# Optimization experiments

Measured on AMD Instinct MI355X. Metric: run time of the kernel, lower is better.

Reference implementation:

```python
import jax, jax.numpy as jnp
import numpy as np

BATCH, T, IN, HID = 64, 2048, 128, 256

def setup_inputs() -> dict:
    key = jax.random.key(0)
    ks = jax.random.split(key, 6)
    s = 0.05
    return {
        "x": jax.random.normal(ks[0], (BATCH, T, IN), dtype=jnp.float32),
        "w_ih0": jax.random.normal(ks[1], (IN, 4 * HID), dtype=jnp.float32) * s,
        "w_hh0": jax.random.normal(ks[2], (HID, 4 * HID), dtype=jnp.float32) * s,
        "b0": jnp.zeros((4 * HID,), dtype=jnp.float32),
        "w_ih1": jax.random.normal(ks[3], (HID, 4 * HID), dtype=jnp.float32) * s,
        "w_hh1": jax.random.normal(ks[4], (HID, 4 * HID), dtype=jnp.float32) * s,
        "b1": jnp.zeros((4 * HID,), dtype=jnp.float32),
    }

def _run_layer(xs, h0, c0, w_ih, w_hh, b):
    # xs: [T, B, D]. Original code iterates input_[T-1-t], i.e. reversed time.
    def step(carry, xt):
        h, c = carry
        gates = xt @ w_ih + h @ w_hh + b            # [B, 4H]
        f, i, o, g = jnp.split(gates, 4, axis=1)     # split order f,i,o,g as in source
        c1 = jax.nn.sigmoid(f) * c + jax.nn.sigmoid(i) * jnp.tanh(g)
        h1 = jax.nn.sigmoid(o) * jnp.tanh(c1)
        return (h1, c1), h1
    (hT, cT), ys = jax.lax.scan(step, (h0, c0), xs[::-1])
    return ys, hT, cT

def reference(x, w_ih0, w_hh0, b0, w_ih1, w_hh1, b1):
    xs = jnp.transpose(x, (1, 0, 2))                 # batch_first -> [T, B, IN]
    B = xs.shape[1]
    H = w_hh0.shape[0]
    h0 = jnp.zeros((B, H), dtype=xs.dtype)
    # Both layers start from the SAME zero hx (faithful to source).
    y0, hn0, cn0 = _run_layer(xs, h0, h0, w_ih0, w_hh0, b0)
    y1, hn1, cn1 = _run_layer(y0, h0, h0, w_ih1, w_hh1, b1)
    # Source never transposes output back: output is [T, B, H]
    return y1, (jnp.stack([hn0, hn1], 0), jnp.stack([cn0, cn1], 0))
```

## Files before the change

kernel.cpp:

```cpp
#include <hip/hip_runtime.h>
#include <cstdint>
#include <cstddef>

#define T_STEPS 2048
#define NBATCH  64
#define HID     256
#define NGATE   1024

#define REC_LDS_BYTES (128*1024 + 8192 + 1024)

typedef _Float16 f16x8 __attribute__((ext_vector_type(8)));
typedef _Float16 h2f   __attribute__((ext_vector_type(2)));
typedef float    f32x4 __attribute__((ext_vector_type(4)));
typedef unsigned short u16x4 __attribute__((ext_vector_type(4)));

__device__ __forceinline__ unsigned short f2h_bits(float f) {
    _Float16 h = (_Float16)f;
    return __builtin_bit_cast(unsigned short, h);
}
__device__ __forceinline__ float h2f_scalar(unsigned short u) {
    return (float)__builtin_bit_cast(_Float16, u);
}

__device__ __forceinline__ float fdot2u(unsigned int hh, unsigned int ww, float acc) {
#if __has_builtin(__builtin_amdgcn_fdot2)
    return __builtin_amdgcn_fdot2(__builtin_bit_cast(h2f, hh),
                                  __builtin_bit_cast(h2f, ww), acc, false);
#else
    h2f a = __builtin_bit_cast(h2f, hh), b = __builtin_bit_cast(h2f, ww);
    return acc + (float)a.x * (float)b.x + (float)a.y * (float)b.y;
#endif
}

#define OFF_G    ((size_t)0)
#define OFF_Y0   ((size_t)268435456)
#define OFF_RW0  ((size_t)335544320)
#define OFF_RW1  ((size_t)335937536)
#define OFF_LF0  ((size_t)336330752)
#define OFF_LF1  ((size_t)336461824)
#define OFF_BS0  ((size_t)336592896)
#define OFF_BS1  ((size_t)336855040)
#define WS_NEED  ((size_t)337379328)

__global__ void convert_weights(const float* __restrict__ w_ih0, const float* __restrict__ w_hh0,
                                const float* __restrict__ w_ih1, const float* __restrict__ w_hh1,
                                unsigned short* __restrict__ RW0, unsigned short* __restrict__ RW1,
                                unsigned short* __restrict__ LF0, unsigned short* __restrict__ LF1,
                                unsigned short* __restrict__ BS0, unsigned short* __restrict__ BS1)
{
    int gid = blockIdx.x * blockDim.x + threadIdx.x;
    int gsz = gridDim.x * blockDim.x;
    for (int s = gid; s < 196608; s += gsz) {
        int i = s & 7;
        int t = s >> 3;
        int slot = t & 511;
        int q = t >> 9;
        int g = q / 12, c = q % 12;
        int l = slot & 63, wv = slot >> 6;
        int kh = wv & 1, ug = wv >> 1;
        int jp = c * 4 + (i >> 1);
        int k = kh * 128 + jp * 2 + (i & 1);
        int col = g * 256 + ug * 64 + l;
        RW0[s] = f2h_bits(w_hh0[k * 1024 + col]);
        RW1[s] = f2h_bits(w_hh1[k * 1024 + col]);
    }
    for (int s = gid; s < 65536; s += gsz) {
        int i = s & 7;
        int t = s >> 3;
        int slot = t & 511;
        int r = t >> 9;
        int g = r >> 2, cc = r & 3;
        int l = slot & 63, wv = slot >> 6;
        int kh = wv & 1, ug = wv >> 1;
        int jp = 48 + cc * 4 + (i >> 1);
        int k = kh * 128 + jp * 2 + (i & 1);
        int col = g * 256 + ug * 64 + l;
        LF0[s] = f2h_bits(w_hh0[k * 1024 + col]);
        LF1[s] = f2h_bits(w_hh1[k * 1024 + col]);
    }
    for (int s = gid; s < 131072; s += gsz) {
        int i = s & 7, lane = (s >> 3) & 63, kb = (s >> 9) & 3, n16 = s >> 11;
        int k = kb * 32 + (lane >> 4) * 8 + i;
        int n = n16 * 16 + (lane & 15);
        BS0[s] = f2h_bits(w_ih0[k * 1024 + n]);
    }
    for (int s = gid; s < 262144; s += gsz) {
        int i = s & 7, lane = (s >> 3) & 63, kb = (s >> 9) & 7, n16 = s >> 12;
        int k = kb * 32 + (lane >> 4) * 8 + i;
        int n = n16 * 16 + (lane & 15);
        BS1[s] = f2h_bits(w_ih1[k * 1024 + n]);
    }
}

template <int KB, int LAYER>
__global__ __launch_bounds__(256) void gemm_in(const float* __restrict__ A32,
                                               const unsigned short* __restrict__ A16,
                                               const unsigned short* __restrict__ Bsw,
                                               const float* __restrict__ bias,
                                               unsigned short* __restrict__ Gout)
{
    const int lane = threadIdx.x & 63;
    const int wave = threadIdx.x >> 6;
    const int nblk = blockIdx.x & 15;
    const int rblk = blockIdx.x >> 4;
    const int r0 = rblk * 128 + wave * 32;
    const int quad = lane >> 4, ln = lane & 15;

    f32x4 acc[2][4];
#pragma unroll
    for (int q = 0; q < 4; q++) {
        float bv = bias[(nblk * 4 + q) * 16 + ln];
#pragma unroll
        for (int mt = 0; mt < 2; mt++) {
            acc[mt][q][0] = bv; acc[mt][q][1] = bv; acc[mt][q][2] = bv; acc[mt][q][3] = bv;
        }
    }
    const int ar0 = r0 + ln, ar1 = r0 + 16 + ln;
    size_t aoff0, aoff1;
    if (LAYER == 0) {
        aoff0 = ((size_t)(ar0 & 63) * 2048 + (size_t)(2047 - (ar0 >> 6))) * 128;
        aoff1 = ((size_t)(ar1 & 63) * 2048 + (size_t)(2047 - (ar1 >> 6))) * 128;
    } else {
        aoff0 = ((size_t)(2047 - (ar0 >> 6)) * 64 + (size_t)(ar0 & 63)) * 256;
        aoff1 = ((size_t)(2047 - (ar1 >> 6)) * 64 + (size_t)(ar1 & 63)) * 256;
    }
#pragma unroll
    for (int kb = 0; kb < KB; kb++) {
        const int k0 = kb * 32 + quad * 8;
        f16x8 a0, a1;
        if (LAYER == 0) {
            const float* p0 = A32 + aoff0 + k0;
            const float* p1 = A32 + aoff1 + k0;
            float4 fa = *(const float4*)(p0);
            float4 fb = *(const float4*)(p0 + 4);
            float4 fc = *(const float4*)(p1);
            float4 fd = *(const float4*)(p1 + 4);
            a0[0] = (_Float16)fa.x; a0[1] = (_Float16)fa.y; a0[2] = (_Float16)fa.z; a0[3] = (_Float16)fa.w;
            a0[4] = (_Float16)fb.x; a0[5] = (_Float16)fb.y; a0[6] = (_Float16)fb.z; a0[7] = (_Float16)fb.w;
            a1[0] = (_Float16)fc.x; a1[1] = (_Float16)fc.y; a1[2] = (_Float16)fc.z; a1[3] = (_Float16)fc.w;
            a1[4] = (_Float16)fd.x; a1[5] = (_Float16)fd.y; a1[6] = (_Float16)fd.z; a1[7] = (_Float16)fd.w;
        } else {
            a0 = *(const f16x8*)(A16 + aoff0 + k0);
            a1 = *(const f16x8*)(A16 + aoff1 + k0);
        }
#pragma unroll
        for (int q = 0; q < 4; q++) {
            f16x8 bq = *(const f16x8*)(Bsw + (((size_t)(nblk * 4 + q) * KB + kb) * 64 + lane) * 8);
            acc[0][q] = __builtin_amdgcn_mfma_f32_16x16x32_f16(a0, bq, acc[0][q], 0, 0, 0);
            acc[1][q] = __builtin_amdgcn_mfma_f32_16x16x32_f16(a1, bq, acc[1][q], 0, 0, 0);
        }
    }
#pragma unroll
    for (int mt = 0; mt < 2; mt++)
#pragma unroll
        for (int q = 0; q < 4; q++)
#pragma unroll
            for (int rg = 0; rg < 4; rg++) {
                int row = r0 + mt * 16 + quad * 4 + rg;
                int col = (nblk * 4 + q) * 16 + ln;
                int swz = ((col & 255) << 2) | (col >> 8);
                Gout[(size_t)row * 1024 + swz] = f2h_bits(acc[mt][q][rg]);
            }
}

template <int LAYER>
__global__ __launch_bounds__(512, 2) void lstm_rec(const unsigned short* __restrict__ G,
                                                   const unsigned short* __restrict__ RW,
                                                   const unsigned short* __restrict__ LF,
                                                   unsigned short* __restrict__ Y0,
                                                   float* __restrict__ Out)
{
    extern __shared__ char smem[];
    uint4*  lds_w  = (uint4*)smem;
    float4* pb     = (float4*)(smem + 131072);
    unsigned short* lds_h0 = (unsigned short*)(smem + 131072 + 8192);
    unsigned short* lds_h1 = lds_h0 + 256;

    const int b = blockIdx.x;
    const int tid = threadIdx.x;
    const int wv = tid >> 6, l = tid & 63;
    const int kh = wv & 1;
    const int ug = wv >> 1;
    const int m = ug * 64 + l;

    uint4 rw[4][12];
#pragma unroll
    for (int g = 0; g < 4; ++g)
#pragma unroll
        for (int c = 0; c < 12; ++c)
            rw[g][c] = *(const uint4*)(RW + ((size_t)((g * 12 + c) * 512) + tid) * 8);

    {
        const uint4* src = (const uint4*)LF;
        for (int i = tid; i < 8192; i += 512) lds_w[i] = src[i];
    }
    if (tid < 256) lds_h0[tid] = 0;
    float c_state = 0.f, hprev = 0.f;
    __syncthreads();

    const u16x4* Gp = (const u16x4*)G;
    const size_t gbase = (size_t)b * 256 + m;
    u16x4 gp = Gp[gbase];

    for (int t = 0; t < T_STEPS; ++t) {
        const uint4* hv4 = (const uint4*)((t & 1) ? lds_h1 : lds_h0);
        uint4 hq = hv4[kh * 16 + (l & 15)];

        const int tn = (t + 1 < T_STEPS) ? t + 1 : t;
        u16x4 gpn = Gp[(size_t)tn * 16384 + gbase];

        if (t && kh == 0) {
            if (LAYER == 0) Y0[((size_t)(t - 1) * 64 + b) * 256 + m] = f2h_bits(hprev);
            else            Out[((size_t)(t - 1) * 64 + b) * 256 + m] = hprev;
        }

        unsigned hx = hq.x, hy = hq.y, hz = hq.z, hw = hq.w;
        unsigned sh[64];
#pragma unroll
        for (int q = 0; q < 16; ++q) {
            sh[q * 4 + 0] = __builtin_amdgcn_readlane(hx, q);
            sh[q * 4 + 1] = __builtin_amdgcn_readlane(hy, q);
            sh[q * 4 + 2] = __builtin_amdgcn_readlane(hz, q);
            sh[q * 4 + 3] = __builtin_amdgcn_readlane(hw, q);
        }

        float acc[4] = {0.f, 0.f, 0.f, 0.f};
#pragma unroll
        for (int c = 0; c < 12; ++c) {
#pragma unroll
            for (int g = 0; g < 4; ++g) {
                uint4 w = rw[g][c];
                acc[g] = fdot2u(sh[c * 4 + 0], w.x, acc[g]);
                acc[g] = fdot2u(sh[c * 4 + 1], w.y, acc[g]);
                acc[g] = fdot2u(sh[c * 4 + 2], w.z, acc[g]);
                acc[g] = fdot2u(sh[c * 4 + 3], w.w, acc[g]);
            }
        }
#pragma unroll
        for (int cc = 0; cc < 4; ++cc) {
#pragma unroll
            for (int g = 0; g < 4; ++g) {
                uint4 w = lds_w[(g * 4 + cc) * 512 + tid];
                acc[g] = fdot2u(sh[48 + cc * 4 + 0], w.x, acc[g]);
                acc[g] = fdot2u(sh[48 + cc * 4 + 1], w.y, acc[g]);
                acc[g] = fdot2u(sh[48 + cc * 4 + 2], w.z, acc[g]);
                acc[g] = fdot2u(sh[48 + cc * 4 + 3], w.w, acc[g]);
            }
        }

        float4 pv; pv.x = acc[0]; pv.y = acc[1]; pv.z = acc[2]; pv.w = acc[3];
        pb[tid] = pv;
        __syncthreads();
        float4 pp = pb[tid ^ 64];

        float fg = h2f_scalar(gp[0]) + (acc[0] + pp.x);
        float ig = h2f_scalar(gp[1]) + (acc[1] + pp.y);
        float og = h2f_scalar(gp[2]) + (acc[2] + pp.z);
        float gg = h2f_scalar(gp[3]) + (acc[3] + pp.w);

        float sf = 1.f / (1.f + __expf(-fg));
        float si = 1.f / (1.f + __expf(-ig));
        float so = 1.f / (1.f + __expf(-og));
        float tg = 1.f - 2.f / (1.f + __expf(2.f * gg));
        c_state = sf * c_state + si * tg;
        float tc = 1.f - 2.f / (1.f + __expf(2.f * c_state));
        float h = so * tc;
        hprev = h;

        unsigned short* hn = (t & 1) ? lds_h0 : lds_h1;
        if (kh == 0) hn[m] = f2h_bits(h);
        gp = gpn;
        __syncthreads();
    }
    if (kh == 0) {
        if (LAYER == 0) Y0[((size_t)(T_STEPS - 1) * 64 + b) * 256 + m] = f2h_bits(hprev);
        else            Out[((size_t)(T_STEPS - 1) * 64 + b) * 256 + m] = hprev;
        Out[(size_t)33554432 + (size_t)LAYER * 16384 + (size_t)b * 256 + m] = hprev;
        Out[(size_t)33554432 + 32768 + (size_t)LAYER * 16384 + (size_t)b * 256 + m] = c_state;
    }
}

extern "C" void kernel_launch(void* const* d_in, const int* in_sizes, int n_in,
                              void* d_out, int out_size, void* d_ws, size_t ws_size,
                              hipStream_t stream)
{
    const float* x     = (const float*)d_in[0];
    const float* w_ih0 = (const float*)d_in[1];
    const float* w_hh0 = (const float*)d_in[2];
    const float* b0    = (const float*)d_in[3];
    const float* w_ih1 = (const float*)d_in[4];
    const float* w_hh1 = (const float*)d_in[5];
    const float* b1    = (const float*)d_in[6];
    float* out = (float*)d_out;

    if (ws_size < WS_NEED) return;

    char* ws = (char*)d_ws;
    unsigned short* G   = (unsigned short*)(ws + OFF_G);
    unsigned short* Y0  = (unsigned short*)(ws + OFF_Y0);
    unsigned short* RW0 = (unsigned short*)(ws + OFF_RW0);
    unsigned short* RW1 = (unsigned short*)(ws + OFF_RW1);
    unsigned short* LF0 = (unsigned short*)(ws + OFF_LF0);
    unsigned short* LF1 = (unsigned short*)(ws + OFF_LF1);
    unsigned short* BS0 = (unsigned short*)(ws + OFF_BS0);
    unsigned short* BS1 = (unsigned short*)(ws + OFF_BS1);

    (void)hipFuncSetAttribute(reinterpret_cast<const void*>(&lstm_rec<0>),
                              hipFuncAttributeMaxDynamicSharedMemorySize, REC_LDS_BYTES);
    (void)hipFuncSetAttribute(reinterpret_cast<const void*>(&lstm_rec<1>),
                              hipFuncAttributeMaxDynamicSharedMemorySize, REC_LDS_BYTES);

    convert_weights<<<1024, 256, 0, stream>>>(w_ih0, w_hh0, w_ih1, w_hh1,
                                              RW0, RW1, LF0, LF1, BS0, BS1);
    gemm_in<4, 0><<<16384, 256, 0, stream>>>(x, nullptr, BS0, b0, G);
    lstm_rec<0><<<64, 512, REC_LDS_BYTES, stream>>>(G, RW0, LF0, Y0, out);
    gemm_in<8, 1><<<16384, 256, 0, stream>>>(nullptr, Y0, BS1, b1, G);
    lstm_rec<1><<<64, 512, REC_LDS_BYTES, stream>>>(G, RW1, LF1, Y0, out);
}
```

Measured before the change: 7.957 ms.

## Stream recurrent weight tail from global/L2 instead of LDS and remap gate columns

Reorganizes the recurrent weight layout so each lane covers two hidden units with paired gates, with the two halves of the gate set exchanged by a cross-lane shuffle. The weight tail that did not fit in registers moves out of LDS. It is now reloaded from global memory (L2-resident) every step in a double-buffered prefetch, which removes the 128KB LDS footprint. The hidden vector is read directly from LDS as uint4 instead of broadcast via readlane into scalar registers. The aim is to cut LDS usage and the readlane SALU overhead. The cost is per-step global loads on the serial critical path and extra shuffles.

```diff
diff --git a/kernel.cpp b/kernel.cpp
--- a/kernel.cpp
+++ b/kernel.cpp
@@ -7,12 +7,11 @@
 #define HID     256
 #define NGATE   1024
 
-#define REC_LDS_BYTES (128*1024 + 8192 + 1024)
+#define REC_LDS_BYTES (8192 + 1024)
 
 typedef _Float16 f16x8 __attribute__((ext_vector_type(8)));
 typedef _Float16 h2f   __attribute__((ext_vector_type(2)));
 typedef float    f32x4 __attribute__((ext_vector_type(4)));
-typedef unsigned short u16x4 __attribute__((ext_vector_type(4)));
 
 __device__ __forceinline__ unsigned short f2h_bits(float f) {
     _Float16 h = (_Float16)f;
@@ -34,49 +33,52 @@
 
 #define OFF_G    ((size_t)0)
 #define OFF_Y0   ((size_t)268435456)
-#define OFF_RW0  ((size_t)335544320)
-#define OFF_RW1  ((size_t)335937536)
-#define OFF_LF0  ((size_t)336330752)
-#define OFF_LF1  ((size_t)336461824)
+#define OFF_WR0  ((size_t)335544320)
+#define OFF_WR1  ((size_t)335872000)
+#define OFF_WG0  ((size_t)336199680)
+#define OFF_WG1  ((size_t)336396288)
 #define OFF_BS0  ((size_t)336592896)
 #define OFF_BS1  ((size_t)336855040)
 #define WS_NEED  ((size_t)337379328)
 
 __global__ void convert_weights(const float* __restrict__ w_ih0, const float* __restrict__ w_hh0,
                                 const float* __restrict__ w_ih1, const float* __restrict__ w_hh1,
-                                unsigned short* __restrict__ RW0, unsigned short* __restrict__ RW1,
-                                unsigned short* __restrict__ LF0, unsigned short* __restrict__ LF1,
+                                unsigned short* __restrict__ WR0, unsigned short* __restrict__ WR1,
+                                unsigned short* __restrict__ WG0, unsigned short* __restrict__ WG1,
                                 unsigned short* __restrict__ BS0, unsigned short* __restrict__ BS1)
 {
     int gid = blockIdx.x * blockDim.x + threadIdx.x;
     int gsz = gridDim.x * blockDim.x;
-    for (int s = gid; s < 196608; s += gsz) {
+    for (int s = gid; s < 163840; s += gsz) {
         int i = s & 7;
         int t = s >> 3;
         int slot = t & 511;
-        int q = t >> 9;
-        int g = q / 12, c = q % 12;
+        int ci = t >> 9;
+        int cx = ci / 10, c = ci % 10;
         int l = slot & 63, wv = slot >> 6;
-        int kh = wv & 1, ug = wv >> 1;
-        int jp = c * 4 + (i >> 1);
-        int k = kh * 128 + jp * 2 + (i & 1);
-        int col = g * 256 + ug * 64 + l;
-        RW0[s] = f2h_bits(w_hh0[k * 1024 + col]);
-        RW1[s] = f2h_bits(w_hh1[k * 1024 + col]);
-    }
-    for (int s = gid; s < 65536; s += gsz) {
+        int kh = wv & 1, lw = wv >> 1;
+        int upper = l >> 5, lu = l & 31;
+        int unit = lw * 64 + lu + ((cx >= 2) ? 32 : 0);
+        int j = unit + upper * 512 + (cx & 1) * 256;
+        int k = kh * 128 + (c * 4 + (i >> 1)) * 2 + (i & 1);
+        WR0[s] = f2h_bits(w_hh0[k * 1024 + j]);
+        WR1[s] = f2h_bits(w_hh1[k * 1024 + j]);
+    }
+    for (int s = gid; s < 98304; s += gsz) {
         int i = s & 7;
         int t = s >> 3;
         int slot = t & 511;
-        int r = t >> 9;
-        int g = r >> 2, cc = r & 3;
+        int ti = t >> 9;
+        int cx = ti / 6, cc = ti % 6;
+        int c = 10 + cc;
         int l = slot & 63, wv = slot >> 6;
-        int kh = wv & 1, ug = wv >> 1;
-        int jp = 48 + cc * 4 + (i >> 1);
-        int k = kh * 128 + jp * 2 + (i & 1);
-        int col = g * 256 + ug * 64 + l;
-        LF0[s] = f2h_bits(w_hh0[k * 1024 + col]);
-        LF1[s] = f2h_bits(w_hh1[k * 1024 + col]);
+        int kh = wv & 1, lw = wv >> 1;
+        int upper = l >> 5, lu = l & 31;
+        int unit = lw * 64 + lu + ((cx >= 2) ? 32 : 0);
+        int j = unit + upper * 512 + (cx & 1) * 256;
+        int k = kh * 128 + (c * 4 + (i >> 1)) * 2 + (i & 1);
+        WG0[s] = f2h_bits(w_hh0[k * 1024 + j]);
+        WG1[s] = f2h_bits(w_hh1[k * 1024 + j]);
     }
     for (int s = gid; s < 131072; s += gsz) {
         int i = s & 7, lane = (s >> 3) & 63, kb = (s >> 9) & 3, n16 = s >> 11;
@@ -165,118 +167,192 @@
 
 template <int LAYER>
 __global__ __launch_bounds__(512, 2) void lstm_rec(const unsigned short* __restrict__ G,
-                                                   const unsigned short* __restrict__ RW,
-                                                   const unsigned short* __restrict__ LF,
+                                                   const unsigned short* __restrict__ WR,
+                                                   const unsigned short* __restrict__ WG,
                                                    unsigned short* __restrict__ Y0,
                                                    float* __restrict__ Out)
 {
     extern __shared__ char smem[];
-    uint4*  lds_w  = (uint4*)smem;
-    float4* pb     = (float4*)(smem + 131072);
-    unsigned short* lds_h0 = (unsigned short*)(smem + 131072 + 8192);
+    float4* pb = (float4*)smem;
+    unsigned short* lds_h0 = (unsigned short*)(smem + 8192);
     unsigned short* lds_h1 = lds_h0 + 256;
 
     const int b = blockIdx.x;
     const int tid = threadIdx.x;
     const int wv = tid >> 6, l = tid & 63;
     const int kh = wv & 1;
-    const int ug = wv >> 1;
-    const int m = ug * 64 + l;
-
-    uint4 rw[4][12];
-#pragma unroll
-    for (int g = 0; g < 4; ++g)
-#pragma unroll
-        for (int c = 0; c < 12; ++c)
-            rw[g][c] = *(const uint4*)(RW + ((size_t)((g * 12 + c) * 512) + tid) * 8);
-
-    {
-        const uint4* src = (const uint4*)LF;
-        for (int i = tid; i < 8192; i += 512) lds_w[i] = src[i];
-    }
+    const int lw = wv >> 1;
+    const int upper = l >> 5, lu = l & 31;
+    const int u0 = lw * 64 + lu;
+    const int u1 = u0 + 32;
+
+    uint4 wr[4][10];
+#pragma unroll
+    for (int cx = 0; cx < 4; ++cx)
+#pragma unroll
+        for (int c = 0; c < 10; ++c)
+            wr[cx][c] = *(const uint4*)(WR + ((size_t)((cx * 10 + c) * 512) + tid) * 8);
+
+    const uint4* WGp = (const uint4*)WG;
+
     if (tid < 256) lds_h0[tid] = 0;
-    float c_state = 0.f, hprev = 0.f;
+    float c0s = 0.f, c1s = 0.f, hp0 = 0.f, hp1 = 0.f;
     __syncthreads();
 
-    const u16x4* Gp = (const u16x4*)G;
-    const size_t gbase = (size_t)b * 256 + m;
-    u16x4 gp = Gp[gbase];
+    const unsigned int* Gb = (const unsigned int*)G + (size_t)b * 512;
+    const int gi0 = u0 * 2 + upper, gi1 = u1 * 2 + upper;
+    unsigned int gp0 = Gb[gi0];
+    unsigned int gp1 = Gb[gi1];
 
     for (int t = 0; t < T_STEPS; ++t) {
+        const int tn = (t + 1 < T_STEPS) ? t + 1 : t;
+        unsigned int gp0n = Gb[(size_t)tn * 32768 + gi0];
+        unsigned int gp1n = Gb[(size_t)tn * 32768 + gi1];
+
+        uint4 tg0[4], tg1[4];
+#pragma unroll
+        for (int cx = 0; cx < 4; ++cx) tg0[cx] = WGp[(cx * 6 + 0) * 512 + tid];
+#pragma unroll
+        for (int cx = 0; cx < 4; ++cx) tg1[cx] = WGp[(cx * 6 + 1) * 512 + tid];
+
+        if (t && kh == 0 && upper == 0) {
+            if (LAYER == 0) {
+                Y0[((size_t)(t - 1) * 64 + b) * 256 + u0] = f2h_bits(hp0);
+                Y0[((size_t)(t - 1) * 64 + b) * 256 + u1] = f2h_bits(hp1);
+            } else {
+                Out[((size_t)(t - 1) * 64 + b) * 256 + u0] = hp0;
+                Out[((size_t)(t - 1) * 64 + b) * 256 + u1] = hp1;
+            }
+        }
+
         const uint4* hv4 = (const uint4*)((t & 1) ? lds_h1 : lds_h0);
-        uint4 hq = hv4[kh * 16 + (l & 15)];
-
-        const int tn = (t + 1 < T_STEPS) ? t + 1 : t;
-        u16x4 gpn = Gp[(size_t)tn * 16384 + gbase];
-
-        if (t && kh == 0) {
-            if (LAYER == 0) Y0[((size_t)(t - 1) * 64 + b) * 256 + m] = f2h_bits(hprev);
-            else            Out[((size_t)(t - 1) * 64 + b) * 256 + m] = hprev;
-        }
-
-        unsigned hx = hq.x, hy = hq.y, hz = hq.z, hw = hq.w;
-        unsigned sh[64];
-#pragma unroll
-        for (int q = 0; q < 16; ++q) {
-            sh[q * 4 + 0] = __builtin_amdgcn_readlane(hx, q);
-            sh[q * 4 + 1] = __builtin_amdgcn_readlane(hy, q);
-            sh[q * 4 + 2] = __builtin_amdgcn_readlane(hz, q);
-            sh[q * 4 + 3] = __builtin_amdgcn_readlane(hw, q);
-        }
-
-        float acc[4] = {0.f, 0.f, 0.f, 0.f};
-#pragma unroll
-        for (int c = 0; c < 12; ++c) {
-#pragma unroll
-            for (int g = 0; g < 4; ++g) {
-                uint4 w = rw[g][c];
-                acc[g] = fdot2u(sh[c * 4 + 0], w.x, acc[g]);
-                acc[g] = fdot2u(sh[c * 4 + 1], w.y, acc[g]);
-                acc[g] = fdot2u(sh[c * 4 + 2], w.z, acc[g]);
-                acc[g] = fdot2u(sh[c * 4 + 3], w.w, acc[g]);
+        float a0 = 0.f, a1 = 0.f, a2 = 0.f, a3 = 0.f;
+
+#pragma unroll
+        for (int c = 0; c < 10; ++c) {
+            uint4 h4 = hv4[kh * 16 + c];
+            uint4 w;
+            w = wr[0][c];
+            a0 = fdot2u(h4.x, w.x, a0); a0 = fdot2u(h4.y, w.y, a0);
+            a0 = fdot2u(h4.z, w.z, a0); a0 = fdot2u(h4.w, w.w, a0);
+            w = wr[1][c];
+            a1 = fdot2u(h4.x, w.x, a1); a1 = fdot2u(h4.y, w.y, a1);
+            a1 = fdot2u(h4.z, w.z, a1); a1 = fdot2u(h4.w, w.w, a1);
+            w = wr[2][c];
+            a2 = fdot2u(h4.x, w.x, a2); a2 = fdot2u(h4.y, w.y, a2);
+            a2 = fdot2u(h4.z, w.z, a2); a2 = fdot2u(h4.w, w.w, a2);
+            w = wr[3][c];
+            a3 = fdot2u(h4.x, w.x, a3); a3 = fdot2u(h4.y, w.y, a3);
+            a3 = fdot2u(h4.z, w.z, a3); a3 = fdot2u(h4.w, w.w, a3);
+        }
+#pragma unroll
+        for (int cc = 0; cc < 6; ++cc) {
+            const int c = 10 + cc;
+            uint4 h4 = hv4[kh * 16 + c];
+            if ((cc & 1) == 0) {
+                uint4 w;
+                w = tg0[0];
+                a0 = fdot2u(h4.x, w.x, a0); a0 = fdot2u(h4.y, w.y, a0);
+                a0 = fdot2u(h4.z, w.z, a0); a0 = fdot2u(h4.w, w.w, a0);
+                w = tg0[1];
+                a1 = fdot2u(h4.x, w.x, a1); a1 = fdot2u(h4.y, w.y, a1);
+                a1 = fdot2u(h4.z, w.z, a1); a1 = fdot2u(h4.w, w.w, a1);
+                w = tg0[2];
+                a2 = fdot2u(h4.x, w.x, a2); a2 = fdot2u(h4.y, w.y, a2);
+                a2 = fdot2u(h4.z, w.z, a2); a2 = fdot2u(h4.w, w.w, a2);
+                w = tg0[3];
+                a3 = fdot2u(h4.x, w.x, a3); a3 = fdot2u(h4.y, w.y, a3);
+                a3 = fdot2u(h4.z, w.z, a3); a3 = fdot2u(h4.w, w.w, a3);
+                if (cc + 2 < 6) {
+#pragma unroll
+                    for (int cx = 0; cx < 4; ++cx)
+                        tg0[cx] = WGp[(cx * 6 + cc + 2) * 512 + tid];
+                }
+            } else {
+                uint4 w;
+                w = tg1[0];
+                a0 = fdot2u(h4.x, w.x, a0); a0 = fdot2u(h4.y, w.y, a0);
+                a0 = fdot2u(h4.z, w.z, a0); a0 = fdot2u(h4.w, w.w, a0);
+                w = tg1[1];
+                a1 = fdot2u(h4.x, w.x, a1); a1 = fdot2u(h4.y, w.y, a1);
+                a1 = fdot2u(h4.z, w.z, a1); a1 = fdot2u(h4.w, w.w, a1);
+                w = tg1[2];
+                a2 = fdot2u(h4.x, w.x, a2); a2 = fdot2u(h4.y, w.y, a2);
+                a2 = fdot2u(h4.z, w.z, a2); a2 = fdot2u(h4.w, w.w, a2);
+                w = tg1[3];
+                a3 = fdot2u(h4.x, w.x, a3); a3 = fdot2u(h4.y, w.y, a3);
+                a3 = fdot2u(h4.z, w.z, a3); a3 = fdot2u(h4.w, w.w, a3);
+                if (cc + 2 < 6) {
+#pragma unroll
+                    for (int cx = 0; cx < 4; ++cx)
+                        tg1[cx] = WGp[(cx * 6 + cc + 2) * 512 + tid];
+                }
             }
         }
-#pragma unroll
-        for (int cc = 0; cc < 4; ++cc) {
-#pragma unroll
-            for (int g = 0; g < 4; ++g) {
-                uint4 w = lds_w[(g * 4 + cc) * 512 + tid];
-                acc[g] = fdot2u(sh[48 + cc * 4 + 0], w.x, acc[g]);
-                acc[g] = fdot2u(sh[48 + cc * 4 + 1], w.y, acc[g]);
-                acc[g] = fdot2u(sh[48 + cc * 4 + 2], w.z, acc[g]);
-                acc[g] = fdot2u(sh[48 + cc * 4 + 3], w.w, acc[g]);
-            }
-        }
-
-        float4 pv; pv.x = acc[0]; pv.y = acc[1]; pv.z = acc[2]; pv.w = acc[3];
+
+        float4 pv; pv.x = a0; pv.y = a1; pv.z = a2; pv.w = a3;
         pb[tid] = pv;
         __syncthreads();
         float4 pp = pb[tid ^ 64];
 
-        float fg = h2f_scalar(gp[0]) + (acc[0] + pp.x);
-        float ig = h2f_scalar(gp[1]) + (acc[1] + pp.y);
-        float og = h2f_scalar(gp[2]) + (acc[2] + pp.z);
-        float gg = h2f_scalar(gp[3]) + (acc[3] + pp.w);
-
-        float sf = 1.f / (1.f + __expf(-fg));
-        float si = 1.f / (1.f + __expf(-ig));
-        float so = 1.f / (1.f + __expf(-og));
-        float tg = 1.f - 2.f / (1.f + __expf(2.f * gg));
-        c_state = sf * c_state + si * tg;
-        float tc = 1.f - 2.f / (1.f + __expf(2.f * c_state));
-        float h = so * tc;
-        hprev = h;
+        float s0 = a0 + pp.x, s1 = a1 + pp.y;
+        float s2 = a2 + pp.z, s3 = a3 + pp.w;
+
+        {
+            float v0 = h2f_scalar((unsigned short)(gp0 & 0xffff)) + s0;
+            float v1 = h2f_scalar((unsigned short)(gp0 >> 16)) + s1;
+            float q0 = __shfl_xor(v0, 32, 64);
+            float q1 = __shfl_xor(v1, 32, 64);
+            float fg = upper ? q0 : v0;
+            float ig = upper ? q1 : v1;
+            float og = upper ? v0 : q0;
+            float gg = upper ? v1 : q1;
+            float sf = 1.f / (1.f + __expf(-fg));
+            float si = 1.f / (1.f + __expf(-ig));
+            float so = 1.f / (1.f + __expf(-og));
+            float tg = 1.f - 2.f / (1.f + __expf(2.f * gg));
+            c0s = sf * c0s + si * tg;
+            float tc = 1.f - 2.f / (1.f + __expf(2.f * c0s));
+            hp0 = so * tc;
+        }
+        {
+            float v0 = h2f_scalar((unsigned short)(gp1 & 0xffff)) + s2;
+            float v1 = h2f_scalar((unsigned short)(gp1 >> 16)) + s3;
+            float q0 = __shfl_xor(v0, 32, 64);
+            float q1 = __shfl_xor(v1, 32, 64);
+            float fg = upper ? q0 : v0;
+            float ig = upper ? q1 : v1;
+            float og = upper ? v0 : q0;
+            float gg = upper ? v1 : q1;
+            float sf = 1.f / (1.f + __expf(-fg));
+            float si = 1.f / (1.f + __expf(-ig));
+            float so = 1.f / (1.f + __expf(-og));
+            float tg = 1.f - 2.f / (1.f + __expf(2.f * gg));
+            c1s = sf * c1s + si * tg;
+            float tc = 1.f - 2.f / (1.f + __expf(2.f * c1s));
+            hp1 = so * tc;
+        }
 
         unsigned short* hn = (t & 1) ? lds_h0 : lds_h1;
-        if (kh == 0) hn[m] = f2h_bits(h);
-        gp = gpn;
+        if (kh == 0 && upper == 0) {
+            hn[u0] = f2h_bits(hp0);
+            hn[u1] = f2h_bits(hp1);
+        }
+        gp0 = gp0n; gp1 = gp1n;
         __syncthreads();
     }
-    if (kh == 0) {
-        if (LAYER == 0) Y0[((size_t)(T_STEPS - 1) * 64 + b) * 256 + m] = f2h_bits(hprev);
-        else            Out[((size_t)(T_STEPS - 1) * 64 + b) * 256 + m] = hprev;
-        Out[(size_t)33554432 + (size_t)LAYER * 16384 + (size_t)b * 256 + m] = hprev;
-        Out[(size_t)33554432 + 32768 + (size_t)LAYER * 16384 + (size_t)b * 256 + m] = c_state;
+    if (kh == 0 && upper == 0) {
+        if (LAYER == 0) {
+            Y0[((size_t)(T_STEPS - 1) * 64 + b) * 256 + u0] = f2h_bits(hp0);
+            Y0[((size_t)(T_STEPS - 1) * 64 + b) * 256 + u1] = f2h_bits(hp1);
+        } else {
+            Out[((size_t)(T_STEPS - 1) * 64 + b) * 256 + u0] = hp0;
+            Out[((size_t)(T_STEPS - 1) * 64 + b) * 256 + u1] = hp1;
+        }
+        Out[(size_t)33554432 + (size_t)LAYER * 16384 + (size_t)b * 256 + u0] = hp0;
+        Out[(size_t)33554432 + (size_t)LAYER * 16384 + (size_t)b * 256 + u1] = hp1;
+        Out[(size_t)33554432 + 32768 + (size_t)LAYER * 16384 + (size_t)b * 256 + u0] = c0s;
+        Out[(size_t)33554432 + 32768 + (size_t)LAYER * 16384 + (size_t)b * 256 + u1] = c1s;
     }
 }
 
@@ -298,10 +374,10 @@
     char* ws = (char*)d_ws;
     unsigned short* G   = (unsigned short*)(ws + OFF_G);
     unsigned short* Y0  = (unsigned short*)(ws + OFF_Y0);
-    unsigned short* RW0 = (unsigned short*)(ws + OFF_RW0);
-    unsigned short* RW1 = (unsigned short*)(ws + OFF_RW1);
-    unsigned short* LF0 = (unsigned short*)(ws + OFF_LF0);
-    unsigned short* LF1 = (unsigned short*)(ws + OFF_LF1);
+    unsigned short* WR0 = (unsigned short*)(ws + OFF_WR0);
+    unsigned short* WR1 = (unsigned short*)(ws + OFF_WR1);
+    unsigned short* WG0 = (unsigned short*)(ws + OFF_WG0);
+    unsigned short* WG1 = (unsigned short*)(ws + OFF_WG1);
     unsigned short* BS0 = (unsigned short*)(ws + OFF_BS0);
     unsigned short* BS1 = (unsigned short*)(ws + OFF_BS1);
 
@@ -311,9 +387,9 @@
                               hipFuncAttributeMaxDynamicSharedMemorySize, REC_LDS_BYTES);
 
     convert_weights<<<1024, 256, 0, stream>>>(w_ih0, w_hh0, w_ih1, w_hh1,
-                                              RW0, RW1, LF0, LF1, BS0, BS1);
+                                              WR0, WR1, WG0, WG1, BS0, BS1);
     gemm_in<4, 0><<<16384, 256, 0, stream>>>(x, nullptr, BS0, b0, G);
-    lstm_rec<0><<<64, 512, REC_LDS_BYTES, stream>>>(G, RW0, LF0, Y0, out);
+    lstm_rec<0><<<64, 512, REC_LDS_BYTES, stream>>>(G, WR0, WG0, Y0, out);
     gemm_in<8, 1><<<16384, 256, 0, stream>>>(nullptr, Y0, BS1, b1, G);
-    lstm_rec<1><<<64, 512, REC_LDS_BYTES, stream>>>(G, RW1, LF1, Y0, out);
-}
+    lstm_rec<1><<<64, 512, REC_LDS_BYTES, stream>>>(G, WR1, WG1, Y0, out);
+}
```

Result: slower. 17.38 ms (+118.4%).

## Halve recurrent block to 256 threads with 8 gate columns per thread

Applied to the files above, without the earlier changes.

Restructures the recurrent LSTM kernel from 512 to 256 threads per block. Each thread now computes partial dot products for two hidden units (8 gate columns) over half of K. It holds twice as many weights in registers (8x12 uint4) and reads h directly from LDS as uint4 instead of broadcasting via readlane. The partial sums are exchanged through two LDS buffers and every thread finishes one unit. This aims to cut per-step readlane overhead and give every thread output work, at the cost of much higher register pressure with one wave per SIMD, and twice the LDS weight reads per thread.

```diff
diff --git a/kernel.cpp b/kernel.cpp
--- a/kernel.cpp
+++ b/kernel.cpp
@@ -7,6 +7,7 @@
 #define HID     256
 #define NGATE   1024
 
+#define RC 12
 #define REC_LDS_BYTES (128*1024 + 8192 + 1024)
 
 typedef _Float16 f16x8 __attribute__((ext_vector_type(8)));
@@ -34,8 +35,8 @@
 
 #define OFF_G    ((size_t)0)
 #define OFF_Y0   ((size_t)268435456)
-#define OFF_RW0  ((size_t)335544320)
-#define OFF_RW1  ((size_t)335937536)
+#define OFF_WR0  ((size_t)335544320)
+#define OFF_WR1  ((size_t)335937536)
 #define OFF_LF0  ((size_t)336330752)
 #define OFF_LF1  ((size_t)336461824)
 #define OFF_BS0  ((size_t)336592896)
@@ -44,7 +45,7 @@
 
 __global__ void convert_weights(const float* __restrict__ w_ih0, const float* __restrict__ w_hh0,
                                 const float* __restrict__ w_ih1, const float* __restrict__ w_hh1,
-                                unsigned short* __restrict__ RW0, unsigned short* __restrict__ RW1,
+                                unsigned short* __restrict__ WR0, unsigned short* __restrict__ WR1,
                                 unsigned short* __restrict__ LF0, unsigned short* __restrict__ LF1,
                                 unsigned short* __restrict__ BS0, unsigned short* __restrict__ BS1)
 {
@@ -53,30 +54,32 @@
     for (int s = gid; s < 196608; s += gsz) {
         int i = s & 7;
         int t = s >> 3;
-        int slot = t & 511;
-        int q = t >> 9;
-        int g = q / 12, c = q % 12;
-        int l = slot & 63, wv = slot >> 6;
-        int kh = wv & 1, ug = wv >> 1;
-        int jp = c * 4 + (i >> 1);
-        int k = kh * 128 + jp * 2 + (i & 1);
-        int col = g * 256 + ug * 64 + l;
-        RW0[s] = f2h_bits(w_hh0[k * 1024 + col]);
-        RW1[s] = f2h_bits(w_hh1[k * 1024 + col]);
+        int tid = t & 255;
+        int ci = t >> 8;
+        int c = ci % 12, cx = ci / 12;
+        int gate = cx & 3, us = cx >> 2;
+        int wv = tid >> 6, l = tid & 63;
+        int kh = wv >> 1, ug = wv & 1;
+        int unit = ug * 128 + us * 64 + l;
+        int j = gate * 256 + unit;
+        int k = kh * 128 + (c * 4 + (i >> 1)) * 2 + (i & 1);
+        WR0[s] = f2h_bits(w_hh0[k * 1024 + j]);
+        WR1[s] = f2h_bits(w_hh1[k * 1024 + j]);
     }
     for (int s = gid; s < 65536; s += gsz) {
         int i = s & 7;
         int t = s >> 3;
-        int slot = t & 511;
-        int r = t >> 9;
-        int g = r >> 2, cc = r & 3;
-        int l = slot & 63, wv = slot >> 6;
-        int kh = wv & 1, ug = wv >> 1;
-        int jp = 48 + cc * 4 + (i >> 1);
-        int k = kh * 128 + jp * 2 + (i & 1);
-        int col = g * 256 + ug * 64 + l;
-        LF0[s] = f2h_bits(w_hh0[k * 1024 + col]);
-        LF1[s] = f2h_bits(w_hh1[k * 1024 + col]);
+        int tid = t & 255;
+        int idx = t >> 8;
+        int cc = idx & 3, cx = idx >> 2;
+        int gate = cx & 3, us = cx >> 2;
+        int wv = tid >> 6, l = tid & 63;
+        int kh = wv >> 1, ug = wv & 1;
+        int unit = ug * 128 + us * 64 + l;
+        int j = gate * 256 + unit;
+        int k = kh * 128 + ((12 + cc) * 4 + (i >> 1)) * 2 + (i & 1);
+        LF0[s] = f2h_bits(w_hh0[k * 1024 + j]);
+        LF1[s] = f2h_bits(w_hh1[k * 1024 + j]);
     }
     for (int s = gid; s < 131072; s += gsz) {
         int i = s & 7, lane = (s >> 3) & 63, kb = (s >> 9) & 3, n16 = s >> 11;
@@ -164,120 +167,151 @@
 }
 
 template <int LAYER>
-__global__ __launch_bounds__(512, 2) void lstm_rec(const unsigned short* __restrict__ G,
-                                                   const unsigned short* __restrict__ RW,
+__global__ __launch_bounds__(256, 1) void lstm_rec(const unsigned short* __restrict__ G,
+                                                   const unsigned short* __restrict__ WR,
                                                    const unsigned short* __restrict__ LF,
                                                    unsigned short* __restrict__ Y0,
                                                    float* __restrict__ Out)
 {
     extern __shared__ char smem[];
-    uint4*  lds_w  = (uint4*)smem;
-    float4* pb     = (float4*)(smem + 131072);
+    uint4*  lds_w = (uint4*)smem;
+    float4* pb_a  = (float4*)(smem + 131072);
+    float4* pb_b  = (float4*)(smem + 131072 + 4096);
     unsigned short* lds_h0 = (unsigned short*)(smem + 131072 + 8192);
     unsigned short* lds_h1 = lds_h0 + 256;
 
     const int b = blockIdx.x;
     const int tid = threadIdx.x;
     const int wv = tid >> 6, l = tid & 63;
-    const int kh = wv & 1;
-    const int ug = wv >> 1;
-    const int m = ug * 64 + l;
-
-    uint4 rw[4][12];
-#pragma unroll
-    for (int g = 0; g < 4; ++g)
-#pragma unroll
-        for (int c = 0; c < 12; ++c)
-            rw[g][c] = *(const uint4*)(RW + ((size_t)((g * 12 + c) * 512) + tid) * 8);
+    const int kh = wv >> 1;
+    const int ug = wv & 1;
+    const int mu = ug * 128 + kh * 64 + l;
+
+    uint4 wr[8][RC];
+#pragma unroll
+    for (int cx = 0; cx < 8; ++cx)
+#pragma unroll
+        for (int c = 0; c < RC; ++c)
+            wr[cx][c] = *(const uint4*)(WR + ((size_t)(cx * RC + c) * 256 + tid) * 8);
 
     {
         const uint4* src = (const uint4*)LF;
-        for (int i = tid; i < 8192; i += 512) lds_w[i] = src[i];
-    }
-    if (tid < 256) lds_h0[tid] = 0;
-    float c_state = 0.f, hprev = 0.f;
+        for (int i = tid; i < 8192; i += 256) lds_w[i] = src[i];
+    }
+    lds_h0[tid] = 0;
+    float c_state = 0.f, hlast = 0.f;
     __syncthreads();
 
     const u16x4* Gp = (const u16x4*)G;
-    const size_t gbase = (size_t)b * 256 + m;
+    const size_t gbase = (size_t)b * 256 + mu;
     u16x4 gp = Gp[gbase];
 
     for (int t = 0; t < T_STEPS; ++t) {
-        const uint4* hv4 = (const uint4*)((t & 1) ? lds_h1 : lds_h0);
-        uint4 hq = hv4[kh * 16 + (l & 15)];
-
         const int tn = (t + 1 < T_STEPS) ? t + 1 : t;
-        u16x4 gpn = Gp[(size_t)tn * 16384 + gbase];
-
-        if (t && kh == 0) {
-            if (LAYER == 0) Y0[((size_t)(t - 1) * 64 + b) * 256 + m] = f2h_bits(hprev);
-            else            Out[((size_t)(t - 1) * 64 + b) * 256 + m] = hprev;
-        }
-
-        unsigned hx = hq.x, hy = hq.y, hz = hq.z, hw = hq.w;
-        unsigned sh[64];
-#pragma unroll
-        for (int q = 0; q < 16; ++q) {
-            sh[q * 4 + 0] = __builtin_amdgcn_readlane(hx, q);
-            sh[q * 4 + 1] = __builtin_amdgcn_readlane(hy, q);
-            sh[q * 4 + 2] = __builtin_amdgcn_readlane(hz, q);
-            sh[q * 4 + 3] = __builtin_amdgcn_readlane(hw, q);
-        }
-
-        float acc[4] = {0.f, 0.f, 0.f, 0.f};
-#pragma unroll
-        for (int c = 0; c < 12; ++c) {
-#pragma unroll
-            for (int g = 0; g < 4; ++g) {
-                uint4 w = rw[g][c];
-                acc[g] = fdot2u(sh[c * 4 + 0], w.x, acc[g]);
-                acc[g] = fdot2u(sh[c * 4 + 1], w.y, acc[g]);
-                acc[g] = fdot2u(sh[c * 4 + 2], w.z, acc[g]);
-                acc[g] = fdot2u(sh[c * 4 + 3], w.w, acc[g]);
-            }
+        u16x4 gn = Gp[(size_t)tn * 16384 + gbase];
+
+        const uint4* hv4 = (const uint4*)((t & 1) ? lds_h1 : lds_h0) + kh * 16;
+
+        float a0 = 0.f, a1 = 0.f, a2 = 0.f, a3 = 0.f;
+        float a4 = 0.f, a5 = 0.f, a6 = 0.f, a7 = 0.f;
+
+#pragma unroll
+        for (int c = 0; c < RC; ++c) {
+            uint4 h4 = hv4[c];
+            uint4 w;
+            w = wr[0][c];
+            a0 = fdot2u(h4.x, w.x, a0); a0 = fdot2u(h4.y, w.y, a0);
+            a0 = fdot2u(h4.z, w.z, a0); a0 = fdot2u(h4.w, w.w, a0);
+            w = wr[1][c];
+            a1 = fdot2u(h4.x, w.x, a1); a1 = fdot2u(h4.y, w.y, a1);
+            a1 = fdot2u(h4.z, w.z, a1); a1 = fdot2u(h4.w, w.w, a1);
+            w = wr[2][c];
+            a2 = fdot2u(h4.x, w.x, a2); a2 = fdot2u(h4.y, w.y, a2);
+            a2 = fdot2u(h4.z, w.z, a2); a2 = fdot2u(h4.w, w.w, a2);
+            w = wr[3][c];
+            a3 = fdot2u(h4.x, w.x, a3); a3 = fdot2u(h4.y, w.y, a3);
+            a3 = fdot2u(h4.z, w.z, a3); a3 = fdot2u(h4.w, w.w, a3);
+            w = wr[4][c];
+            a4 = fdot2u(h4.x, w.x, a4); a4 = fdot2u(h4.y, w.y, a4);
+            a4 = fdot2u(h4.z, w.z, a4); a4 = fdot2u(h4.w, w.w, a4);
+            w = wr[5][c];
+            a5 = fdot2u(h4.x, w.x, a5); a5 = fdot2u(h4.y, w.y, a5);
+            a5 = fdot2u(h4.z, w.z, a5); a5 = fdot2u(h4.w, w.w, a5);
+            w = wr[6][c];
+            a6 = fdot2u(h4.x, w.x, a6); a6 = fdot2u(h4.y, w.y, a6);
+            a6 = fdot2u(h4.z, w.z, a6); a6 = fdot2u(h4.w, w.w, a6);
+            w = wr[7][c];
+            a7 = fdot2u(h4.x, w.x, a7); a7 = fdot2u(h4.y, w.y, a7);
+            a7 = fdot2u(h4.z, w.z, a7); a7 = fdot2u(h4.w, w.w, a7);
         }
 #pragma unroll
         for (int cc = 0; cc < 4; ++cc) {
-#pragma unroll
-            for (int g = 0; g < 4; ++g) {
-                uint4 w = lds_w[(g * 4 + cc) * 512 + tid];
-                acc[g] = fdot2u(sh[48 + cc * 4 + 0], w.x, acc[g]);
-                acc[g] = fdot2u(sh[48 + cc * 4 + 1], w.y, acc[g]);
-                acc[g] = fdot2u(sh[48 + cc * 4 + 2], w.z, acc[g]);
-                acc[g] = fdot2u(sh[48 + cc * 4 + 3], w.w, acc[g]);
-            }
-        }
-
-        float4 pv; pv.x = acc[0]; pv.y = acc[1]; pv.z = acc[2]; pv.w = acc[3];
-        pb[tid] = pv;
+            uint4 h4 = hv4[RC + cc];
+            uint4 w;
+            w = lds_w[(0 * 4 + cc) * 256 + tid];
+            a0 = fdot2u(h4.x, w.x, a0); a0 = fdot2u(h4.y, w.y, a0);
+            a0 = fdot2u(h4.z, w.z, a0); a0 = fdot2u(h4.w, w.w, a0);
+            w = lds_w[(1 * 4 + cc) * 256 + tid];
+            a1 = fdot2u(h4.x, w.x, a1); a1 = fdot2u(h4.y, w.y, a1);
+            a1 = fdot2u(h4.z, w.z, a1); a1 = fdot2u(h4.w, w.w, a1);
+            w = lds_w[(2 * 4 + cc) * 256 + tid];
+            a2 = fdot2u(h4.x, w.x, a2); a2 = fdot2u(h4.y, w.y, a2);
+            a2 = fdot2u(h4.z, w.z, a2); a2 = fdot2u(h4.w, w.w, a2);
+            w = lds_w[(3 * 4 + cc) * 256 + tid];
+            a3 = fdot2u(h4.x, w.x, a3); a3 = fdot2u(h4.y, w.y, a3);
+            a3 = fdot2u(h4.z, w.z, a3); a3 = fdot2u(h4.w, w.w, a3);
+            w = lds_w[(4 * 4 + cc) * 256 + tid];
+            a4 = fdot2u(h4.x, w.x, a4); a4 = fdot2u(h4.y, w.y, a4);
+            a4 = fdot2u(h4.z, w.z, a4); a4 = fdot2u(h4.w, w.w, a4);
+            w = lds_w[(5 * 4 + cc) * 256 + tid];
+            a5 = fdot2u(h4.x, w.x, a5); a5 = fdot2u(h4.y, w.y, a5);
+            a5 = fdot2u(h4.z, w.z, a5); a5 = fdot2u(h4.w, w.w, a5);
+            w = lds_w[(6 * 4 + cc) * 256 + tid];
+            a6 = fdot2u(h4.x, w.x, a6); a6 = fdot2u(h4.y, w.y, a6);
+            a6 = fdot2u(h4.z, w.z, a6); a6 = fdot2u(h4.w, w.w, a6);
+            w = lds_w[(7 * 4 + cc) * 256 + tid];
+            a7 = fdot2u(h4.x, w.x, a7); a7 = fdot2u(h4.y, w.y, a7);
+            a7 = fdot2u(h4.z, w.z, a7); a7 = fdot2u(h4.w, w.w, a7);
+        }
+
+        float4 pva; pva.x = a0; pva.y = a1; pva.z = a2; pva.w = a3;
+        float4 pvb; pvb.x = a4; pvb.y = a5; pvb.z = a6; pvb.w = a7;
+        pb_a[tid] = pva;
+        pb_b[tid] = pvb;
         __syncthreads();
-        float4 pp = pb[tid ^ 64];
-
-        float fg = h2f_scalar(gp[0]) + (acc[0] + pp.x);
-        float ig = h2f_scalar(gp[1]) + (acc[1] + pp.y);
-        float og = h2f_scalar(gp[2]) + (acc[2] + pp.z);
-        float gg = h2f_scalar(gp[3]) + (acc[3] + pp.w);
-
-        float sf = 1.f / (1.f + __expf(-fg));
-        float si = 1.f / (1.f + __expf(-ig));
-        float so = 1.f / (1.f + __expf(-og));
-        float tg = 1.f - 2.f / (1.f + __expf(2.f * gg));
+        float4 qa = pb_a[tid ^ 128];
+        float4 qb = pb_b[tid ^ 128];
+
+        float sf_, si_, so_, sg_;
+        if (kh == 0) {
+            sf_ = a0 + qa.x; si_ = a1 + qa.y; so_ = a2 + qa.z; sg_ = a3 + qa.w;
+        } else {
+            sf_ = a4 + qb.x; si_ = a5 + qb.y; so_ = a6 + qb.z; sg_ = a7 + qb.w;
+        }
+
+        float vf = h2f_scalar(gp[0]) + sf_;
+        float vi = h2f_scalar(gp[1]) + si_;
+        float vo = h2f_scalar(gp[2]) + so_;
+        float vg = h2f_scalar(gp[3]) + sg_;
+
+        float sf = 1.f / (1.f + __expf(-vf));
+        float si = 1.f / (1.f + __expf(-vi));
+        float so = 1.f / (1.f + __expf(-vo));
+        float tg = 1.f - 2.f / (1.f + __expf(2.f * vg));
         c_state = sf * c_state + si * tg;
         float tc = 1.f - 2.f / (1.f + __expf(2.f * c_state));
         float h = so * tc;
-        hprev = h;
-
-        unsigned short* hn = (t & 1) ? lds_h0 : lds_h1;
-        if (kh == 0) hn[m] = f2h_bits(h);
-        gp = gpn;
+        hlast = h;
+
+        if (LAYER == 0) Y0[((size_t)t * 64 + b) * 256 + mu] = f2h_bits(h);
+        else            Out[((size_t)t * 64 + b) * 256 + mu] = h;
+        ((t & 1) ? lds_h0 : lds_h1)[mu] = f2h_bits(h);
+
+        gp = gn;
         __syncthreads();
     }
-    if (kh == 0) {
-        if (LAYER == 0) Y0[((size_t)(T_STEPS - 1) * 64 + b) * 256 + m] = f2h_bits(hprev);
-        else            Out[((size_t)(T_STEPS - 1) * 64 + b) * 256 + m] = hprev;
-        Out[(size_t)33554432 + (size_t)LAYER * 16384 + (size_t)b * 256 + m] = hprev;
-        Out[(size_t)33554432 + 32768 + (size_t)LAYER * 16384 + (size_t)b * 256 + m] = c_state;
-    }
+    Out[(size_t)33554432 + (size_t)LAYER * 16384 + (size_t)b * 256 + mu] = hlast;
+    Out[(size_t)33554432 + 32768 + (size_t)LAYER * 16384 + (size_t)b * 256 + mu] = c_state;
 }
 
 extern "C" void kernel_launch(void* const* d_in, const int* in_sizes, int n_in,
@@ -298,8 +332,8 @@
     char* ws = (char*)d_ws;
     unsigned short* G   = (unsigned short*)(ws + OFF_G);
     unsigned short* Y0  = (unsigned short*)(ws + OFF_Y0);
-    unsigned short* RW0 = (unsigned short*)(ws + OFF_RW0);
-    unsigned short* RW1 = (unsigned short*)(ws + OFF_RW1);
+    unsigned short* WR0 = (unsigned short*)(ws + OFF_WR0);
+    unsigned short* WR1 = (unsigned short*)(ws + OFF_WR1);
     unsigned short* LF0 = (unsigned short*)(ws + OFF_LF0);
     unsigned short* LF1 = (unsigned short*)(ws + OFF_LF1);
     unsigned short* BS0 = (unsigned short*)(ws + OFF_BS0);
@@ -311,9 +345,9 @@
                               hipFuncAttributeMaxDynamicSharedMemorySize, REC_LDS_BYTES);
 
     convert_weights<<<1024, 256, 0, stream>>>(w_ih0, w_hh0, w_ih1, w_hh1,
-                                              RW0, RW1, LF0, LF1, BS0, BS1);
+                                              WR0, WR1, LF0, LF1, BS0, BS1);
     gemm_in<4, 0><<<16384, 256, 0, stream>>>(x, nullptr, BS0, b0, G);
-    lstm_rec<0><<<64, 512, REC_LDS_BYTES, stream>>>(G, RW0, LF0, Y0, out);
+    lstm_rec<0><<<64, 256, REC_LDS_BYTES, stream>>>(G, WR0, LF0, Y0, out);
     gemm_in<8, 1><<<16384, 256, 0, stream>>>(nullptr, Y0, BS1, b1, G);
-    lstm_rec<1><<<64, 512, REC_LDS_BYTES, stream>>>(G, RW1, LF1, Y0, out);
-}
+    lstm_rec<1><<<64, 256, REC_LDS_BYTES, stream>>>(G, WR1, LF1, Y0, out);
+}
```

Measured after the change: 12.03 ms. +51.2%, slower.
